# Kernel tuning notes

Measured on AMD Instinct MI355X. Metric: run time of the kernel, lower is better.

Reference implementation:

```python
import jax, jax.numpy as jnp
import numpy as np

EPS = 1e-5

def _ln(x, g, b):
    m = x.mean(-1, keepdims=True)
    v = jnp.var(x, axis=-1, keepdims=True)
    return (x - m) * jax.lax.rsqrt(v + EPS) * g + b

def _conv(x, w, b, stride=1, pad=1):
    y = jax.lax.conv_general_dilated(x, w, (stride, stride), [(pad, pad), (pad, pad)],
                                     dimension_numbers=('NCHW', 'OIHW', 'NCHW'))
    return y + b[None, :, None, None]

def _bn(x, g, b, m, v):
    # inference-mode BatchNorm2d
    inv = jax.lax.rsqrt(v + EPS)
    return (x - m[None, :, None, None]) * (g * inv)[None, :, None, None] + b[None, :, None, None]

def _sru_dir(u0, u1, u2, res, vf, vr, bf, br, reverse):
    # elementwise gated recurrence (SRU v2, identity activation, no dropout)
    def step(c, inp):
        a0, a1, a2, rx = inp
        f = jax.nn.sigmoid(a1 + vf * c + bf)
        c2 = f * c + (1.0 - f) * a0
        r = jax.nn.sigmoid(a2 + vr * c2 + br)
        return c2, r * c2 + (1.0 - r) * rx
    c0 = jnp.zeros_like(u0[0])
    _, hs = jax.lax.scan(step, c0, (u0, u1, u2, res), reverse=reverse)
    return hs

def _sru_layer(x, g, b, wp, w, vc, bias, k, h):
    # x: [L,B,n_in]; layer_norm on input, factored weight (projection), bidirectional
    xn = _ln(x, g, b)
    L, B, _ = xn.shape
    U = (xn @ wp) @ w                      # [L,B,2*k*h]
    U = U.reshape(L, B, 2, k, h)
    outs = []
    for d, rev in ((0, False), (1, True)):
        u = U[:, :, d]
        res = u[..., 3, :] if k == 4 else xn[..., d * h:(d + 1) * h]
        outs.append(_sru_dir(u[..., 0, :], u[..., 1, :], u[..., 2, :], res,
                             vc[d, 0], vc[d, 1], bias[d, 0], bias[d, 1], rev))
    return jnp.concatenate(outs, axis=-1)

def _forward(x, conv0_w, conv0_b, rconv1_w, rconv1_b, rbn1_g, rbn1_b, rbn1_m, rbn1_v,
             rconv2_w, rconv2_b, rbn2_g, rbn2_b, rbn2_m, rbn2_v,
             ln0_g, ln0_b, wproj0, w0, vc0, bias0, ln_g, ln_b, wproj, w, vc, bias,
             cln_g, cln_b, cls_w):
    H = 512
    h = _conv(x, conv0_w, conv0_b, stride=2)           # [B,32,F/2,T/2]
    for i in range(3):                                  # 3 residual blocks
        r = h
        h1 = jax.nn.relu(_bn(_conv(h, rconv1_w[i], rconv1_b[i]), rbn1_g[i], rbn1_b[i], rbn1_m[i], rbn1_v[i]))
        h2 = _bn(_conv(h1, rconv2_w[i], rconv2_b[i]), rbn2_g[i], rbn2_b[i], rbn2_m[i], rbn2_v[i])
        h = jax.nn.relu(h2 + r)
    Bb, C, Fr, Tt = h.shape
    s = h.reshape(Bb, C * Fr, Tt).transpose(2, 0, 1)   # [T,B,2048]
    s = _sru_layer(s, ln0_g, ln0_b, wproj0, w0, vc0, bias0, 4, H)  # layer 0: n_in != n_out -> k=4
    for i in range(3):                                  # layers 1..3: n_in == n_out -> k=3
        s = _sru_layer(s, ln_g[i], ln_b[i], wproj[i], w[i], vc[i], bias[i], 3, H)
    s = s.transpose(1, 0, 2)                            # [B,T,1024]
    s = _ln(s, cln_g, cln_b)
    return s @ cls_w                                    # [B,T,30]

def setup_inputs():
    key = jax.random.key(0)
    ks = iter(jax.random.split(key, 32))
    def nrm(shape, scale=1.0):
        return jax.random.normal(next(ks), shape, jnp.float32) * scale
    H, P, F2, D, hb = 512, 256, 2048, 1024, -2.0
    d = {}
    d['x'] = nrm((16, 1, 128, 2048))
    d['conv0_w'] = nrm((32, 1, 3, 3), (2.0 / 9) ** 0.5)
    d['conv0_b'] = jnp.zeros((32,))
    d['rconv1_w'] = nrm((3, 32, 32, 3, 3), (2.0 / (32 * 9)) ** 0.5)
    d['rconv1_b'] = jnp.zeros((3, 32))
    d['rbn1_g'] = jnp.ones((3, 32)); d['rbn1_b'] = jnp.zeros((3, 32))
    d['rbn1_m'] = nrm((3, 32), 0.1); d['rbn1_v'] = jnp.ones((3, 32))
    d['rconv2_w'] = nrm((3, 32, 32, 3, 3), (2.0 / (32 * 9)) ** 0.5)
    d['rconv2_b'] = jnp.zeros((3, 32))
    d['rbn2_g'] = 0.1 * jnp.ones((3, 32)); d['rbn2_b'] = jnp.zeros((3, 32))
    d['rbn2_m'] = nrm((3, 32), 0.1); d['rbn2_v'] = jnp.ones((3, 32))
    d['ln0_g'] = jnp.ones((F2,)); d['ln0_b'] = jnp.zeros((F2,))
    d['wproj0'] = nrm((F2, P), F2 ** -0.5)
    d['w0'] = nrm((P, 2 * 4 * H), P ** -0.5)
    d['vc0'] = nrm((2, 2, H), 0.1)
    d['bias0'] = jnp.zeros((2, 2, H)).at[:, 0].set(hb)
    d['ln_g'] = jnp.ones((3, D)); d['ln_b'] = jnp.zeros((3, D))
    d['wproj'] = nrm((3, D, P), D ** -0.5)
    d['w'] = nrm((3, P, 2 * 3 * H), P ** -0.5)
    d['vc'] = nrm((3, 2, 2, H), 0.1)
    d['bias'] = jnp.zeros((3, 2, 2, H)).at[:, :, 0].set(hb)
    d['cln_g'] = jnp.ones((D,)); d['cln_b'] = jnp.zeros((D,))
    d['cls_w'] = nrm((D, 30), D ** -0.5)
    return d

def reference(x, conv0_w, conv0_b, rconv1_w, rconv1_b, rbn1_g, rbn1_b, rbn1_m, rbn1_v,
              rconv2_w, rconv2_b, rbn2_g, rbn2_b, rbn2_m, rbn2_v,
              ln0_g, ln0_b, wproj0, w0, vc0, bias0, ln_g, ln_b, wproj, w, vc, bias,
              cln_g, cln_b, cls_w):
    return _forward(x, conv0_w, conv0_b, rconv1_w, rconv1_b, rbn1_g, rbn1_b, rbn1_m, rbn1_v,
                    rconv2_w, rconv2_b, rbn2_g, rbn2_b, rbn2_m, rbn2_v,
                    ln0_g, ln0_b, wproj0, w0, vc0, bias0, ln_g, ln_b, wproj, w, vc, bias,
                    cln_g, cln_b, cls_w)
```

## Files before the change

### kernel.cpp

```cpp
#include <hip/hip_runtime.h>
#include <hip/hip_bf16.h>
#include <math.h>

#define DEV __device__ __forceinline__

typedef __attribute__((ext_vector_type(8))) short short8;
typedef __attribute__((ext_vector_type(4))) float floatx4;

DEV float b2f_lo(unsigned u) { return __uint_as_float(u << 16); }
DEV float b2f_hi(unsigned u) { return __uint_as_float(u & 0xffff0000u); }

#if __has_builtin(__builtin_amdgcn_exp2f)
DEV float fexp2_(float x) { return __builtin_amdgcn_exp2f(x); }
#else
DEV float fexp2_(float x) { return exp2f(x); }
#endif
#if __has_builtin(__builtin_amdgcn_rcpf)
DEV float frcp_(float x) { return __builtin_amdgcn_rcpf(x); }
#else
DEV float frcp_(float x) { return 1.f / x; }
#endif

DEV void gl2lds16(const void* g, void* l) {
  __builtin_amdgcn_global_load_lds(
      (const __attribute__((address_space(1))) unsigned int*)g,
      (__attribute__((address_space(3))) unsigned int*)l, 16, 0, 0);
}

union U8 { uint4 u; __hip_bfloat16 h[8]; };

DEV int swz64(int x)    { return (x & ~63) | ((x & 15) << 2) | ((x >> 4) & 3); }
DEV int invswz64(int x) { return (x & ~63) | ((x & 3) << 4) | ((x >> 2) & 15); }

__global__ __launch_bounds__(256) void conv_stem_nhwc(const float* __restrict__ x,
    const float* __restrict__ w, const float* __restrict__ bias,
    __hip_bfloat16* __restrict__ out) {
  __shared__ float sX[3][2052];
  __shared__ float sW[288];
  __shared__ float sB[32];
  const int tid = threadIdx.x;
  const int f = blockIdx.x, n = blockIdx.y;
  const float* xb = x + (size_t)n * 262144;

  for (int i = tid; i < 1536; i += 256) {
    int r = i >> 9, c4 = i & 511;
    int fi = 2 * f - 1 + r;
    float4 v = {0.f, 0.f, 0.f, 0.f};
    if (fi >= 0 && fi < 128) v = *(const float4*)&xb[fi * 2048 + c4 * 4];
    sX[r][1 + c4 * 4 + 0] = v.x;
    sX[r][1 + c4 * 4 + 1] = v.y;
    sX[r][1 + c4 * 4 + 2] = v.z;
    sX[r][1 + c4 * 4 + 3] = v.w;
  }
  if (tid < 3) { sX[tid][0] = 0.f; sX[tid][2049] = 0.f; }
  for (int i = tid; i < 288; i += 256) sW[i] = w[i];
  if (tid < 32) sB[tid] = bias[tid];
  __syncthreads();

  float xv[4][9];
#pragma unroll
  for (int q = 0; q < 4; ++q) {
    int t = tid + q * 256;
#pragma unroll
    for (int r = 0; r < 3; ++r)
#pragma unroll
      for (int dc = 0; dc < 3; ++dc)
        xv[q][r * 3 + dc] = sX[r][2 * t + dc];
  }
#pragma unroll
  for (int ocq = 0; ocq < 4; ++ocq) {
    float wr[8][9];
#pragma unroll
    for (int oo = 0; oo < 8; ++oo)
#pragma unroll
      for (int qq = 0; qq < 9; ++qq)
        wr[oo][qq] = sW[(ocq * 8 + oo) * 9 + qq];
#pragma unroll
    for (int q = 0; q < 4; ++q) {
      U8 o;
#pragma unroll
      for (int oo = 0; oo < 8; ++oo) {
        float acc = sB[ocq * 8 + oo];
#pragma unroll
        for (int qq = 0; qq < 9; ++qq) acc = fmaf(wr[oo][qq], xv[q][qq], acc);
        o.h[oo] = __float2bfloat16(acc);
      }
      int t = tid + q * 256;
      *(uint4*)&out[(((size_t)n * 64 + f) * 1024 + t) * 32 + ocq * 8] = o.u;
    }
  }
}

__global__ __launch_bounds__(256) void wtap_conv6(const float* __restrict__ w1,
    const float* __restrict__ w2, __hip_bfloat16* __restrict__ out) {
  int i = blockIdx.x * 256 + threadIdx.x;
  if (i < 55296) {
    int b = i / 9216, r = i - b * 9216;
    int layer = b >> 1, which = b & 1;
    const float* src = (which ? w2 : w1) + layer * 9216;
    int tap = r >> 10, oc = (r >> 5) & 31, ic = r & 31;
    out[b * 9216 + r] = __float2bfloat16(src[(oc * 32 + ic) * 9 + tap]);
  }
}

template <int ADD>
__global__ __launch_bounds__(256) void conv_mfma(const __hip_bfloat16* __restrict__ Hin,
    const __hip_bfloat16* __restrict__ wt,
    const float* __restrict__ cb, const float* __restrict__ bg,
    const float* __restrict__ bb, const float* __restrict__ bm,
    const float* __restrict__ bv, __hip_bfloat16* Hres) {
  __shared__ __hip_bfloat16 sIn[6 * 66 * 40];
  __hip_bfloat16* sOut = sIn;
  const int tid = threadIdx.x;
  const int tb = blockIdx.x, fb = blockIdx.y, n = blockIdx.z;
  const int t0 = tb * 64, f0 = fb * 4;
  const __hip_bfloat16* Hb = Hin + (size_t)n * 2097152;

  for (int c = tid; c < 1584; c += 256) {
    int rr = c / 264;
    int r2 = c - rr * 264;
    int p = r2 >> 2, icq = r2 & 3;
    int fi = f0 - 1 + rr;
    int tg = t0 + p - 1;
    uint4 v = {0, 0, 0, 0};
    if (fi >= 0 && fi < 64 && tg >= 0 && tg < 1024)
      v = *(const uint4*)&Hb[((size_t)fi * 1024 + tg) * 32 + icq * 8];
    *(uint4*)&sIn[(rr * 66 + p) * 40 + icq * 8] = v;
  }

  const int lane = tid & 63, wave = tid >> 6;
  const int fr = lane & 15, fq = lane >> 4;
  short8 bfrag[9][2];
#pragma unroll
  for (int tap = 0; tap < 9; ++tap)
#pragma unroll
    for (int j = 0; j < 2; ++j)
      bfrag[tap][j] = *(const short8*)&wt[(tap * 32 + j * 16 + fr) * 32 + fq * 8];

  __syncthreads();

  const int tw = wave * 16;
  floatx4 acc[4][2];
#pragma unroll
  for (int fp = 0; fp < 4; ++fp)
#pragma unroll
    for (int j = 0; j < 2; ++j) acc[fp][j] = (floatx4){0.f, 0.f, 0.f, 0.f};

#pragma unroll
  for (int fp = 0; fp < 4; ++fp) {
    int pbase = tw + fr;
#pragma unroll
    for (int df = 0; df < 3; ++df)
#pragma unroll
      for (int dc = 0; dc < 3; ++dc) {
        short8 af =
            *(const short8*)&sIn[((fp + df) * 66 + pbase + dc) * 40 + fq * 8];
        acc[fp][0] = __builtin_amdgcn_mfma_f32_16x16x32_bf16(
            af, bfrag[df * 3 + dc][0], acc[fp][0], 0, 0, 0);
        acc[fp][1] = __builtin_amdgcn_mfma_f32_16x16x32_bf16(
            af, bfrag[df * 3 + dc][1], acc[fp][1], 0, 0, 0);
      }
  }

  float sc0 = bg[fr] * rsqrtf(bv[fr] + 1e-5f);
  float sh0 = (cb[fr] - bm[fr]) * sc0 + bb[fr];
  float sc1 = bg[fr + 16] * rsqrtf(bv[fr + 16] + 1e-5f);
  float sh1 = (cb[fr + 16] - bm[fr + 16]) * sc1 + bb[fr + 16];

  __syncthreads();
#pragma unroll
  for (int fp = 0; fp < 4; ++fp)
#pragma unroll
    for (int j = 0; j < 2; ++j) {
      float sc = j ? sc1 : sc0, sh = j ? sh1 : sh0;
#pragma unroll
      for (int reg = 0; reg < 4; ++reg) {
        int t_l = tw + fq * 4 + reg;
        sOut[(fp * 64 + t_l) * 40 + j * 16 + fr] =
            __float2bfloat16(acc[fp][j][reg] * sc + sh);
      }
    }
  __syncthreads();

  for (int c = tid; c < 1024; c += 256) {
    int fp = c >> 8, rem = c & 255;
    int t_l = rem >> 2, icq = rem & 3;
    U8 y;
    y.u = *(uint4*)&sOut[(fp * 64 + t_l) * 40 + icq * 8];
    size_t addr = (((size_t)n * 64 + f0 + fp) * 1024 + t0 + t_l) * 32 + icq * 8;
    U8 o;
    if (ADD) {
      U8 r;
      r.u = *(const uint4*)&Hres[addr];
#pragma unroll
      for (int i = 0; i < 8; ++i)
        o.h[i] = __float2bfloat16(
            fmaxf(__bfloat162float(y.h[i]) + __bfloat162float(r.h[i]), 0.f));
    } else {
#pragma unroll
      for (int i = 0; i < 8; ++i)
        o.h[i] = __float2bfloat16(fmaxf(__bfloat162float(y.h[i]), 0.f));
    }
    *(uint4*)&Hres[addr] = o.u;
  }
}

__global__ __launch_bounds__(256) void ln_nhwc(const __hip_bfloat16* __restrict__ H,
    const float* __restrict__ g, const float* __restrict__ b,
    __hip_bfloat16* __restrict__ xn) {
  int r = blockIdx.x;
  int t = r >> 4, n = r & 15;
  int tid = threadIdx.x;
  int f = tid >> 2, icq = tid & 3;
  U8 v;
  v.u = *(const uint4*)&H[(((size_t)n * 64 + f) * 1024 + t) * 32 + icq * 8];
  float xv[8];
  float sum = 0.f, ss = 0.f;
#pragma unroll
  for (int i = 0; i < 8; ++i) {
    xv[i] = __bfloat162float(v.h[i]);
    sum += xv[i];
    ss += xv[i] * xv[i];
  }
#pragma unroll
  for (int off = 32; off > 0; off >>= 1) {
    sum += __shfl_down(sum, off);
    ss  += __shfl_down(ss, off);
  }
  __shared__ float red[8];
  int lane = tid & 63, wave = tid >> 6;
  if (lane == 0) { red[wave] = sum; red[4 + wave] = ss; }
  __syncthreads();
  sum = red[0] + red[1] + red[2] + red[3];
  ss  = red[4] + red[5] + red[6] + red[7];
  float mean = sum * (1.f / 2048.f);
  float var = ss * (1.f / 2048.f) - mean * mean;
  float inv = rsqrtf(var + 1e-5f);
  U8 o;
#pragma unroll
  for (int i = 0; i < 8; ++i) {
    int cf = (icq * 8 + i) * 64 + f;
    o.h[i] = __float2bfloat16((xv[i] - mean) * inv * g[cf] + b[cf]);
  }
  *(uint4*)&xn[(size_t)r * 2048 + tid * 8] = o.u;
}

__global__ __launch_bounds__(256) void wt_perm0(const float* __restrict__ in,
    __hip_bfloat16* __restrict__ out) {
  int i = blockIdx.x * 256 + threadIdx.x;
  int p = i >> 11, kp = i & 2047;
  int ic = kp & 31, f = kp >> 5;
  out[i] = __float2bfloat16(in[(ic * 64 + f) * 256 + p]);
}

__global__ __launch_bounds__(256) void wt_bf16(const float* __restrict__ in,
    __hip_bfloat16* __restrict__ out, int K, int N, int inStride, int outStride) {
  __shared__ float tile[32][33];
  int x = threadIdx.x, y0 = threadIdx.y;
  int bn = blockIdx.x * 32;
  int bk = blockIdx.y * 32;
  const float* src = in + (size_t)blockIdx.z * inStride;
  __hip_bfloat16* dst = out + (size_t)blockIdx.z * outStride;
#pragma unroll
  for (int i = 0; i < 4; ++i) {
    int yy = y0 + i * 8;
    tile[yy][x] = src[(size_t)(bk + yy) * N + bn + x];
  }
  __syncthreads();
#pragma unroll
  for (int i = 0; i < 4; ++i) {
    int yy = y0 + i * 8;
    dst[(size_t)(bn + yy) * K + bk + x] = __float2bfloat16(tile[x][yy]);
  }
}

__global__ void wexp_prep(const float* __restrict__ in,
    __hip_bfloat16* __restrict__ out, int korig, int inStride, int outStride) {
  __shared__ float tile[32][33];
  int jt = blockIdx.x;
  int ckt = blockIdx.y;
  int z = blockIdx.z;
  int layer = z >> 3, dk = z & 7;
  int d = dk >> 2, k = dk & 3;
  if (k >= korig) return;
  const float* src = in + (size_t)layer * inStride;
  __hip_bfloat16* dst = out + (size_t)layer * outStride;
  int x = threadIdx.x, y0 = threadIdx.y;
#pragma unroll
  for (int i = 0; i < 4; ++i) {
    int yy = y0 + i * 8;
    tile[yy][x] = src[(size_t)(ckt * 32 + yy) * (korig * 1024) +
                      (d * korig + k) * 512 + jt * 32 + x];
  }
  __syncthreads();
#pragma unroll
  for (int i = 0; i < 4; ++i) {
    int yy = y0 + i * 8;
    int ch = d * 512 + jt * 32 + yy;
    int rOld;
    if (korig == 4)
      rOld = (k < 2) ? (ch * 2 + k) : (2048 + ch * 2 + (k - 2));
    else
      rOld = (k < 2) ? (ch * 2 + k) : (2048 + ch);
    int rNew = invswz64(rOld);
    int ckp = swz64(ckt * 32 + x);
    dst[(size_t)rNew * 256 + ckp] = __float2bfloat16(tile[x][yy]);
  }
}

__global__ __launch_bounds__(256) void colsb_prep(const float* __restrict__ bias0,
    const float* __restrict__ bias3, float2* __restrict__ out) {
  int i = blockIdx.x * 256 + threadIdx.x;
  if (i >= 13312) return;
  const float NL2E = -1.44269504f;
  float s = 1.f, bb = 0.f;
  if (i < 4096) {
    int col = i;
    if (col < 2048) {
      int ch = col >> 1, e = col & 1;
      int d = ch >> 9, jj = ch & 511;
      if (e) { s = NL2E; bb = NL2E * bias0[d * 1024 + jj]; }
    } else {
      int cc = col - 2048, ch = cc >> 1, e = cc & 1;
      int d = ch >> 9, jj = ch & 511;
      if (!e) { s = NL2E; bb = NL2E * bias0[d * 1024 + 512 + jj]; }
    }
  } else {
    int rem = i - 4096;
    int layer = rem / 3072, col = rem - layer * 3072;
    const float* bsrc = bias3 + layer * 2048;
    if (col < 2048) {
      int ch = col >> 1, e = col & 1;
      int d = ch >> 9, jj = ch & 511;
      if (e) { s = NL2E; bb = NL2E * bsrc[d * 1024 + jj]; }
    } else {
      int ch = col - 2048;
      int d = ch >> 9, jj = ch & 511;
      s = NL2E; bb = NL2E * bsrc[d * 1024 + 512 + jj];
    }
  }
  out[i] = make_float2(s, bb);
}

__global__ __launch_bounds__(256) void wct_prep(const float* __restrict__ in,
    __hip_bfloat16* __restrict__ out) {
  int i = blockIdx.x * 256 + threadIdx.x;
  int nn = i >> 10, kk = i & 1023;
  out[i] = __float2bfloat16(nn < 30 ? in[kk * 30 + nn] : 0.f);
}

__global__ __launch_bounds__(256) void gemm_bf16(const __hip_bfloat16* __restrict__ A,
    const __hip_bfloat16* __restrict__ Bt, __hip_bfloat16* __restrict__ C,
    const float2* __restrict__ csb, int M, int N, int K) {
  __shared__ __hip_bfloat16 As[128 * 32];
  __shared__ __hip_bfloat16 Bs[128 * 32];
  const int tid = threadIdx.x;
  const int gx = gridDim.x;
  const int nwg = gx * gridDim.y;
  const int bid = blockIdx.y * gx + blockIdx.x;
  const int wgid = (bid & 7) * (nwg >> 3) + (bid >> 3);
  const int m0 = (wgid / gx) * 128, n0 = (wgid % gx) * 128;
  const int lane = tid & 63, wave = tid >> 6;
  const int wm = wave & 1, wn = wave >> 1;
  const int fr = lane & 15, fq = lane >> 4;
  const int srow = lane >> 2, sch = lane & 3;

  const __hip_bfloat16* ga0 = &A[(size_t)(m0 + wave * 32 + srow) * K + sch * 8];
  const __hip_bfloat16* ga1 = ga0 + (size_t)16 * K;
  const __hip_bfloat16* gb0 = &Bt[(size_t)(n0 + wave * 32 + srow) * K + sch * 8];
  const __hip_bfloat16* gb1 = gb0 + (size_t)16 * K;
  __hip_bfloat16* la0 = &As[(wave * 32) * 32];
  __hip_bfloat16* la1 = &As[(wave * 32 + 16) * 32];
  __hip_bfloat16* lb0 = &Bs[(wave * 32) * 32];
  __hip_bfloat16* lb1 = &Bs[(wave * 32 + 16) * 32];

  floatx4 acc[4][4];
#pragma unroll
  for (int i = 0; i < 4; ++i)
#pragma unroll
    for (int j = 0; j < 4; ++j)
      acc[i][j] = (floatx4){0.f, 0.f, 0.f, 0.f};

  for (int k0 = 0; k0 < K; k0 += 32) {
    __syncthreads();
    gl2lds16(ga0 + k0, la0);
    gl2lds16(ga1 + k0, la1);
    gl2lds16(gb0 + k0, lb0);
    gl2lds16(gb1 + k0, lb1);
    __syncthreads();

    short8 af[4], bf_[4];
#pragma unroll
    for (int i = 0; i < 4; ++i) {
      af[i]  = *(const short8*)&As[(wm * 64 + i * 16 + fr) * 32 + fq * 8];
      bf_[i] = *(const short8*)&Bs[(wn * 64 + i * 16 + fr) * 32 + fq * 8];
    }
#pragma unroll
    for (int i = 0; i < 4; ++i)
#pragma unroll
      for (int j = 0; j < 4; ++j)
        acc[i][j] = __builtin_amdgcn_mfma_f32_16x16x32_bf16(af[i], bf_[j],
                                                            acc[i][j], 0, 0, 0);
  }

  const int p0 = n0 + wn * 64 + fr * 4;
  float s0 = 1.f, s1 = 1.f, s2 = 1.f, s3 = 1.f;
  float c0 = 0.f, c1 = 0.f, c2v = 0.f, c3 = 0.f;
  if (csb) {
    float2 t0 = csb[p0], t1 = csb[p0 + 1], t2 = csb[p0 + 2], t3 = csb[p0 + 3];
    s0 = t0.x; c0 = t0.y; s1 = t1.x; c1 = t1.y;
    s2 = t2.x; c2v = t2.y; s3 = t3.x; c3 = t3.y;
  }
#pragma unroll
  for (int i = 0; i < 4; ++i)
#pragma unroll
    for (int reg = 0; reg < 4; ++reg) {
      int row = m0 + wm * 64 + i * 16 + fq * 4 + reg;
      union { uint2 u; __hip_bfloat16 h[4]; } o;
      o.h[0] = __float2bfloat16(fmaf(acc[i][0][reg], s0, c0));
      o.h[1] = __float2bfloat16(fmaf(acc[i][1][reg], s1, c1));
      o.h[2] = __float2bfloat16(fmaf(acc[i][2][reg], s2, c2v));
      o.h[3] = __float2bfloat16(fmaf(acc[i][3][reg], s3, c3));
      *(uint2*)&C[(size_t)row * N + p0] = o.u;
    }
}

__global__ __launch_bounds__(256) void cls_gemm(const __hip_bfloat16* __restrict__ A,
    const __hip_bfloat16* __restrict__ Wct, float* __restrict__ out) {
  const int tid = threadIdx.x;
  const int lane = tid & 63, wave = tid >> 6;
  const int fr = lane & 15, fq = lane >> 4;
  const int m0 = (blockIdx.x * 4 + wave) * 16;
  floatx4 acc[2];
  acc[0] = (floatx4){0.f, 0.f, 0.f, 0.f};
  acc[1] = (floatx4){0.f, 0.f, 0.f, 0.f};
#pragma unroll 4
  for (int k0 = 0; k0 < 1024; k0 += 32) {
    short8 af = *(const short8*)&A[(size_t)(m0 + fr) * 1024 + k0 + fq * 8];
    short8 b0 = *(const short8*)&Wct[(size_t)fr * 1024 + k0 + fq * 8];
    short8 b1 = *(const short8*)&Wct[(size_t)(16 + fr) * 1024 + k0 + fq * 8];
    acc[0] = __builtin_amdgcn_mfma_f32_16x16x32_bf16(af, b0, acc[0], 0, 0, 0);
    acc[1] = __builtin_amdgcn_mfma_f32_16x16x32_bf16(af, b1, acc[1], 0, 0, 0);
  }
#pragma unroll
  for (int j = 0; j < 2; ++j) {
    int col = j * 16 + fr;
    if (col < 30) {
#pragma unroll
      for (int reg = 0; reg < 4; ++reg) {
        int row = m0 + fq * 4 + reg;
        int t = row >> 4, n = row & 15;
        out[(size_t)n * 30720 + t * 30 + col] = acc[j][reg];
      }
    }
  }
}

template <int ROWB>
__global__ __launch_bounds__(64) void scan_c(const __hip_bfloat16* __restrict__ U,
    const float* __restrict__ vc, __hip_bfloat16* __restrict__ c2out) {
  int gid = blockIdx.x * 64 + threadIdx.x;
  int j = gid & 511;
  int n = (gid >> 9) & 15;
  int d = gid >> 13;
  const float NL2E = -1.44269504f;
  float vf2 = NL2E * vc[d * 1024 + j];

  const char* Ub = (const char*)U + (size_t)n * ROWB + (size_t)(d * 512 + j) * 4;
  char* Ob = (char*)c2out + (size_t)n * 2048 + (size_t)(d * 512 + j) * 2;
  const int US = d ? -(16 * ROWB) : (16 * ROWB);
  const int OS = d ? -32768 : 32768;
  int uoff = d ? 1023 * 16 * ROWB : 0;
  int ooff = d ? 1023 * 32768 : 0;

  uint B0[16], B1[16], B2[16], B3[16];
  float c = 0.f;

#define LOADC(UB)                                                         \
  {                                                                       \
    _Pragma("unroll") for (int ss = 0; ss < 16; ++ss) {                   \
      UB[ss] = *(const uint*)(Ub + uoff);                                 \
      uoff += US;                                                         \
    }                                                                     \
  }

#define COMPC(UB)                                                         \
  {                                                                       \
    _Pragma("unroll") for (int ss = 0; ss < 16; ++ss) {                   \
      uint u = UB[ss];                                                    \
      float a0 = b2f_lo(u), a1p = b2f_hi(u);                              \
      float f = frcp_(1.f + fexp2_(fmaf(vf2, c, a1p)));                   \
      c = fmaf(f, c - a0, a0);                                            \
      *(__hip_bfloat16*)(Ob + ooff) = __float2bfloat16(c);                \
      ooff += OS;                                                         \
    }                                                                     \
  }

  LOADC(B0);
  LOADC(B1);
  LOADC(B2);
  for (int cb = 0; cb < 64; cb += 4) {
    LOADC(B3);
    COMPC(B0);
    if (cb + 4 < 64) LOADC(B0);
    COMPC(B1);
    if (cb + 5 < 64) LOADC(B1);
    COMPC(B2);
    if (cb + 6 < 64) LOADC(B2);
    COMPC(B3);
  }
#undef LOADC
#undef COMPC
}

template <int K4>
__global__ __launch_bounds__(256) void yln(const __hip_bfloat16* __restrict__ c2buf,
    const __hip_bfloat16* __restrict__ U, const __hip_bfloat16* __restrict__ xn,
    const float* __restrict__ vc, const float* __restrict__ g,
    const float* __restrict__ b, __hip_bfloat16* __restrict__ outx) {
  int r = blockIdx.x;
  int tid = threadIdx.x;
  int ch0 = tid * 4;
  const float NL2E = -1.44269504f;

  union { ushort4 u; __hip_bfloat16 h[4]; } cv;
  cv.u = *(const ushort4*)&c2buf[(size_t)r * 1024 + ch0];
  float a2p[4], rx[4];
  if (K4) {
    uint4 pr = *(const uint4*)((const char*)U + (size_t)r * 8192 + 4096 + tid * 16);
    uint pp[4] = {pr.x, pr.y, pr.z, pr.w};
#pragma unroll
    for (int i = 0; i < 4; ++i) { a2p[i] = b2f_lo(pp[i]); rx[i] = b2f_hi(pp[i]); }
  } else {
    union { ushort4 u; __hip_bfloat16 h[4]; } av, xv;
    av.u = *(const ushort4*)((const char*)U + (size_t)r * 6144 + 4096 + tid * 8);
    xv.u = *(const ushort4*)&xn[(size_t)r * 1024 + ch0];
#pragma unroll
    for (int i = 0; i < 4; ++i) {
      a2p[i] = __bfloat162float(av.h[i]);
      rx[i]  = __bfloat162float(xv.h[i]);
    }
  }

  int d = ch0 >> 9, j0 = ch0 & 511;
  float y[4], sum = 0.f, ss = 0.f;
#pragma unroll
  for (int i = 0; i < 4; ++i) {
    float vr2 = NL2E * vc[d * 1024 + 512 + j0 + i];
    float cc = __bfloat162float(cv.h[i]);
    float rr = frcp_(1.f + fexp2_(fmaf(vr2, cc, a2p[i])));
    y[i] = fmaf(rr, cc - rx[i], rx[i]);
    sum += y[i];
    ss += y[i] * y[i];
  }
#pragma unroll
  for (int off = 32; off > 0; off >>= 1) {
    sum += __shfl_down(sum, off);
    ss  += __shfl_down(ss, off);
  }
  __shared__ float red[8];
  int lane = tid & 63, wave = tid >> 6;
  if (lane == 0) { red[wave] = sum; red[4 + wave] = ss; }
  __syncthreads();
  sum = red[0] + red[1] + red[2] + red[3];
  ss  = red[4] + red[5] + red[6] + red[7];
  float mean = sum * (1.f / 1024.f);
  float var = ss * (1.f / 1024.f) - mean * mean;
  float inv = rsqrtf(var + 1e-5f);
  float4 gv = *(const float4*)&g[ch0];
  float4 bv = *(const float4*)&b[ch0];
  float gg[4] = {gv.x, gv.y, gv.z, gv.w};
  float bb[4] = {bv.x, bv.y, bv.z, bv.w};
  union { ushort4 u; __hip_bfloat16 h[4]; } o;
#pragma unroll
  for (int i = 0; i < 4; ++i)
    o.h[i] = __float2bfloat16((y[i] - mean) * inv * gg[i] + bb[i]);
  *(ushort4*)&outx[(size_t)r * 1024 + ch0] = o.u;
}

extern "C" void kernel_launch(void* const* d_in, const int* in_sizes, int n_in,
                              void* d_out, int out_size, void* d_ws, size_t ws_size,
                              hipStream_t stream) {
  const float* x        = (const float*)d_in[0];
  const float* conv0_w  = (const float*)d_in[1];
  const float* conv0_b  = (const float*)d_in[2];
  const float* rconv1_w = (const float*)d_in[3];
  const float* rconv1_b = (const float*)d_in[4];
  const float* rbn1_g   = (const float*)d_in[5];
  const float* rbn1_b   = (const float*)d_in[6];
  const float* rbn1_m   = (const float*)d_in[7];
  const float* rbn1_v   = (const float*)d_in[8];
  const float* rconv2_w = (const float*)d_in[9];
  const float* rconv2_b = (const float*)d_in[10];
  const float* rbn2_g   = (const float*)d_in[11];
  const float* rbn2_b   = (const float*)d_in[12];
  const float* rbn2_m   = (const float*)d_in[13];
  const float* rbn2_v   = (const float*)d_in[14];
  const float* ln0_g    = (const float*)d_in[15];
  const float* ln0_b    = (const float*)d_in[16];
  const float* wproj0   = (const float*)d_in[17];
  const float* w0       = (const float*)d_in[18];
  const float* vc0      = (const float*)d_in[19];
  const float* bias0    = (const float*)d_in[20];
  const float* ln_g     = (const float*)d_in[21];
  const float* ln_b     = (const float*)d_in[22];
  const float* wproj    = (const float*)d_in[23];
  const float* w        = (const float*)d_in[24];
  const float* vc       = (const float*)d_in[25];
  const float* bias     = (const float*)d_in[26];
  const float* cln_g    = (const float*)d_in[27];
  const float* cln_b    = (const float*)d_in[28];
  const float* cls_w    = (const float*)d_in[29];
  float* out = (float*)d_out;

  float* Af = (float*)d_ws;
  float* Bf = Af + 33554432;
  __hip_bfloat16* Ah = (__hip_bfloat16*)Af;
  __hip_bfloat16* Bh = (__hip_bfloat16*)Bf;

  __hip_bfloat16* hA     = Ah;
  __hip_bfloat16* hB     = Bh;
  __hip_bfloat16* wt_all = Ah + 62914560;
  __hip_bfloat16* Wp0t   = Ah + 52428800;

  __hip_bfloat16* c2   = Bh;
  __hip_bfloat16* xnc  = Bh + 16777216;
  __hip_bfloat16* xn3  = Bh + 33554432;
  __hip_bfloat16* tmp  = Bh + 50331648;
  __hip_bfloat16* W3p  = Bh + 54525952;
  __hip_bfloat16* W0p  = Bh + 57671680;
  __hip_bfloat16* Wpt3 = Bh + 58720256;
  float2* csb          = (float2*)(Bh + 59506688);
  __hip_bfloat16* xn0  = Bh;
  __hip_bfloat16* U    = Ah;
  __hip_bfloat16* Wct  = Ah;

  const float2* csb4 = csb;
  const float2* csb3 = csb + 4096;

  wtap_conv6<<<216, 256, 0, stream>>>(rconv1_w, rconv2_w, wt_all);
  wt_perm0<<<2048, 256, 0, stream>>>(wproj0, Wp0t);
  wexp_prep<<<dim3(16, 8, 8), dim3(32, 8), 0, stream>>>(w0, W0p, 4, 0, 0);
  wexp_prep<<<dim3(16, 8, 24), dim3(32, 8), 0, stream>>>(w, W3p, 3,
                                                         786432, 786432);
  wt_bf16<<<dim3(8, 32, 3), dim3(32, 8), 0, stream>>>(wproj, Wpt3, 1024, 256,
                                                      262144, 262144);
  colsb_prep<<<52, 256, 0, stream>>>(bias0, bias, csb);

  conv_stem_nhwc<<<dim3(64, 16), 256, 0, stream>>>(x, conv0_w, conv0_b, hA);
  for (int i = 0; i < 3; ++i) {
    conv_mfma<0><<<dim3(16, 16, 16), 256, 0, stream>>>(hA, wt_all + (i * 2) * 9216,
        rconv1_b + i * 32, rbn1_g + i * 32, rbn1_b + i * 32,
        rbn1_m + i * 32, rbn1_v + i * 32, hB);
    conv_mfma<1><<<dim3(16, 16, 16), 256, 0, stream>>>(hB, wt_all + (i * 2 + 1) * 9216,
        rconv2_b + i * 32, rbn2_g + i * 32, rbn2_b + i * 32,
        rbn2_m + i * 32, rbn2_v + i * 32, hA);
  }

  ln_nhwc<<<16384, 256, 0, stream>>>(hA, ln0_g, ln0_b, xn0);
  gemm_bf16<<<dim3(2, 128), 256, 0, stream>>>(xn0, Wp0t, tmp, nullptr,
                                              16384, 256, 2048);
  gemm_bf16<<<dim3(32, 128), 256, 0, stream>>>(tmp, W0p, U, csb4,
                                               16384, 4096, 256);
  scan_c<8192><<<256, 64, 0, stream>>>(U, vc0, c2);
  __hip_bfloat16* xnA = xn3;
  __hip_bfloat16* xnB = xnc;
  yln<1><<<16384, 256, 0, stream>>>(c2, U, nullptr, vc0, ln_g, ln_b, xnA);

  for (int i = 0; i < 3; ++i) {
    gemm_bf16<<<dim3(2, 128), 256, 0, stream>>>(xnA, Wpt3 + i * 262144, tmp,
                                                nullptr, 16384, 256, 1024);
    gemm_bf16<<<dim3(24, 128), 256, 0, stream>>>(tmp, W3p + i * 786432, U,
                                                 csb3 + i * 3072, 16384, 3072, 256);
    scan_c<6144><<<256, 64, 0, stream>>>(U, vc + i * 2048, c2);
    const float* gg = (i < 2) ? (ln_g + (i + 1) * 1024) : cln_g;
    const float* bb = (i < 2) ? (ln_b + (i + 1) * 1024) : cln_b;
    yln<0><<<16384, 256, 0, stream>>>(c2, U, xnA, vc + i * 2048, gg, bb, xnB);
    __hip_bfloat16* sw = xnA; xnA = xnB; xnB = sw;
  }

  wct_prep<<<128, 256, 0, stream>>>(cls_w, Wct);
  cls_gemm<<<256, 256, 0, stream>>>(xnA, Wct, out);
}
```

Measured before the change: 1.035 ms.

## Load GEMM MFMA fragments directly from global memory with register double buffering

The bf16 GEMM no longer stages A and B tiles through LDS with global_load_lds and two barriers per K step. Each wave now loads its MFMA operand fragments straight from global memory into registers, using two register sets so the next K slice is fetched while the current one is multiplied. This removes LDS traffic and block-wide synchronisation. In exchange each fragment is fetched redundantly by the waves that share it, global accesses become 16-byte strided reads across rows, and the loop assumes K is a multiple of 64.

```diff
diff --git a/kernel.cpp b/kernel.cpp
--- a/kernel.cpp
+++ b/kernel.cpp
@@ -20,12 +20,6 @@
 #else
 DEV float frcp_(float x) { return 1.f / x; }
 #endif
-
-DEV void gl2lds16(const void* g, void* l) {
-  __builtin_amdgcn_global_load_lds(
-      (const __attribute__((address_space(1))) unsigned int*)g,
-      (__attribute__((address_space(3))) unsigned int*)l, 16, 0, 0);
-}
 
 union U8 { uint4 u; __hip_bfloat16 h[8]; };
 
@@ -352,8 +346,6 @@
 __global__ __launch_bounds__(256) void gemm_bf16(const __hip_bfloat16* __restrict__ A,
     const __hip_bfloat16* __restrict__ Bt, __hip_bfloat16* __restrict__ C,
     const float2* __restrict__ csb, int M, int N, int K) {
-  __shared__ __hip_bfloat16 As[128 * 32];
-  __shared__ __hip_bfloat16 Bs[128 * 32];
   const int tid = threadIdx.x;
   const int gx = gridDim.x;
   const int nwg = gx * gridDim.y;
@@ -363,16 +355,14 @@
   const int lane = tid & 63, wave = tid >> 6;
   const int wm = wave & 1, wn = wave >> 1;
   const int fr = lane & 15, fq = lane >> 4;
-  const int srow = lane >> 2, sch = lane & 3;
-
-  const __hip_bfloat16* ga0 = &A[(size_t)(m0 + wave * 32 + srow) * K + sch * 8];
-  const __hip_bfloat16* ga1 = ga0 + (size_t)16 * K;
-  const __hip_bfloat16* gb0 = &Bt[(size_t)(n0 + wave * 32 + srow) * K + sch * 8];
-  const __hip_bfloat16* gb1 = gb0 + (size_t)16 * K;
-  __hip_bfloat16* la0 = &As[(wave * 32) * 32];
-  __hip_bfloat16* la1 = &As[(wave * 32 + 16) * 32];
-  __hip_bfloat16* lb0 = &Bs[(wave * 32) * 32];
-  __hip_bfloat16* lb1 = &Bs[(wave * 32 + 16) * 32];
+
+  const __hip_bfloat16* pa[4];
+  const __hip_bfloat16* pb[4];
+#pragma unroll
+  for (int i = 0; i < 4; ++i) {
+    pa[i] = &A[(size_t)(m0 + wm * 64 + i * 16 + fr) * K + fq * 8];
+    pb[i] = &Bt[(size_t)(n0 + wn * 64 + i * 16 + fr) * K + fq * 8];
+  }
 
   floatx4 acc[4][4];
 #pragma unroll
@@ -381,27 +371,32 @@
     for (int j = 0; j < 4; ++j)
       acc[i][j] = (floatx4){0.f, 0.f, 0.f, 0.f};
 
-  for (int k0 = 0; k0 < K; k0 += 32) {
-    __syncthreads();
-    gl2lds16(ga0 + k0, la0);
-    gl2lds16(ga1 + k0, la1);
-    gl2lds16(gb0 + k0, lb0);
-    gl2lds16(gb1 + k0, lb1);
-    __syncthreads();
-
-    short8 af[4], bf_[4];
-#pragma unroll
-    for (int i = 0; i < 4; ++i) {
-      af[i]  = *(const short8*)&As[(wm * 64 + i * 16 + fr) * 32 + fq * 8];
-      bf_[i] = *(const short8*)&Bs[(wn * 64 + i * 16 + fr) * 32 + fq * 8];
-    }
-#pragma unroll
-    for (int i = 0; i < 4; ++i)
-#pragma unroll
-      for (int j = 0; j < 4; ++j)
-        acc[i][j] = __builtin_amdgcn_mfma_f32_16x16x32_bf16(af[i], bf_[j],
-                                                            acc[i][j], 0, 0, 0);
-  }
+  short8 aC[4], bC[4], aN[4], bN[4];
+
+#define LOADF(AA, BB, kk)                                                 \
+  {                                                                       \
+    _Pragma("unroll") for (int i = 0; i < 4; ++i) {                       \
+      AA[i] = *(const short8*)(pa[i] + (kk));                             \
+      BB[i] = *(const short8*)(pb[i] + (kk));                             \
+    }                                                                     \
+  }
+#define MFMA16(AA, BB)                                                    \
+  {                                                                       \
+    _Pragma("unroll") for (int i = 0; i < 4; ++i)                         \
+    _Pragma("unroll") for (int j = 0; j < 4; ++j)                         \
+      acc[i][j] = __builtin_amdgcn_mfma_f32_16x16x32_bf16(                \
+          AA[i], BB[j], acc[i][j], 0, 0, 0);                              \
+  }
+
+  LOADF(aC, bC, 0);
+  for (int k = 0; k < K; k += 64) {
+    LOADF(aN, bN, k + 32);
+    MFMA16(aC, bC);
+    if (k + 64 < K) LOADF(aC, bC, k + 64);
+    MFMA16(aN, bN);
+  }
+#undef LOADF
+#undef MFMA16
 
   const int p0 = n0 + wn * 64 + fr * 4;
   float s0 = 1.f, s1 = 1.f, s2 = 1.f, s3 = 1.f;
```

New measurement: 1.290 ms. +24.6%, slower.

## Double-buffer LDS tiles in bf16 GEMM to overlap global loads with MFMA

Applied to the files above, without the earlier changes.

Splits the GEMM's shared-memory A and B tiles into two buffers. The next K-slice is loaded directly into LDS while the current slice is computed, with vmcnt waits and barriers sequencing the two. This hides global-load latency behind matrix-core work. The cost is twice the LDS per block, which may lower occupancy. The loop also assumes K is a multiple of 64, and relies on hand-placed wait counts being correct.

```diff
diff --git a/kernel.cpp b/kernel.cpp
--- a/kernel.cpp
+++ b/kernel.cpp
@@ -352,8 +352,8 @@
 __global__ __launch_bounds__(256) void gemm_bf16(const __hip_bfloat16* __restrict__ A,
     const __hip_bfloat16* __restrict__ Bt, __hip_bfloat16* __restrict__ C,
     const float2* __restrict__ csb, int M, int N, int K) {
-  __shared__ __hip_bfloat16 As[128 * 32];
-  __shared__ __hip_bfloat16 Bs[128 * 32];
+  __shared__ __hip_bfloat16 As[2][128 * 32];
+  __shared__ __hip_bfloat16 Bs[2][128 * 32];
   const int tid = threadIdx.x;
   const int gx = gridDim.x;
   const int nwg = gx * gridDim.y;
@@ -369,10 +369,8 @@
   const __hip_bfloat16* ga1 = ga0 + (size_t)16 * K;
   const __hip_bfloat16* gb0 = &Bt[(size_t)(n0 + wave * 32 + srow) * K + sch * 8];
   const __hip_bfloat16* gb1 = gb0 + (size_t)16 * K;
-  __hip_bfloat16* la0 = &As[(wave * 32) * 32];
-  __hip_bfloat16* la1 = &As[(wave * 32 + 16) * 32];
-  __hip_bfloat16* lb0 = &Bs[(wave * 32) * 32];
-  __hip_bfloat16* lb1 = &Bs[(wave * 32 + 16) * 32];
+  const int lo0 = (wave * 32) * 32;
+  const int lo1 = (wave * 32 + 16) * 32;
 
   floatx4 acc[4][4];
 #pragma unroll
@@ -381,27 +379,49 @@
     for (int j = 0; j < 4; ++j)
       acc[i][j] = (floatx4){0.f, 0.f, 0.f, 0.f};
 
-  for (int k0 = 0; k0 < K; k0 += 32) {
-    __syncthreads();
-    gl2lds16(ga0 + k0, la0);
-    gl2lds16(ga1 + k0, la1);
-    gl2lds16(gb0 + k0, lb0);
-    gl2lds16(gb1 + k0, lb1);
-    __syncthreads();
-
-    short8 af[4], bf_[4];
-#pragma unroll
-    for (int i = 0; i < 4; ++i) {
-      af[i]  = *(const short8*)&As[(wm * 64 + i * 16 + fr) * 32 + fq * 8];
-      bf_[i] = *(const short8*)&Bs[(wn * 64 + i * 16 + fr) * 32 + fq * 8];
-    }
-#pragma unroll
-    for (int i = 0; i < 4; ++i)
-#pragma unroll
-      for (int j = 0; j < 4; ++j)
-        acc[i][j] = __builtin_amdgcn_mfma_f32_16x16x32_bf16(af[i], bf_[j],
-                                                            acc[i][j], 0, 0, 0);
-  }
+#define STAGE(BUF, kk)                                                    \
+  {                                                                       \
+    gl2lds16(ga0 + (kk), &As[BUF][lo0]);                                  \
+    gl2lds16(ga1 + (kk), &As[BUF][lo1]);                                  \
+    gl2lds16(gb0 + (kk), &Bs[BUF][lo0]);                                  \
+    gl2lds16(gb1 + (kk), &Bs[BUF][lo1]);                                  \
+  }
+#define COMPUTE(BUF)                                                      \
+  {                                                                       \
+    short8 af[4], bf_[4];                                                 \
+    _Pragma("unroll") for (int i = 0; i < 4; ++i) {                       \
+      af[i]  = *(const short8*)&As[BUF][(wm * 64 + i * 16 + fr) * 32 + fq * 8]; \
+      bf_[i] = *(const short8*)&Bs[BUF][(wn * 64 + i * 16 + fr) * 32 + fq * 8]; \
+    }                                                                     \
+    _Pragma("unroll") for (int i = 0; i < 4; ++i)                         \
+      _Pragma("unroll") for (int j = 0; j < 4; ++j)                       \
+        acc[i][j] = __builtin_amdgcn_mfma_f32_16x16x32_bf16(              \
+            af[i], bf_[j], acc[i][j], 0, 0, 0);                           \
+  }
+#define CFENCE asm volatile("" ::: "memory")
+
+  STAGE(0, 0);
+  for (int k0 = 0; k0 < K; k0 += 64) {
+    STAGE(1, k0 + 32);
+    asm volatile("s_waitcnt vmcnt(4)" ::: "memory");
+    __builtin_amdgcn_s_barrier();
+    COMPUTE(0);
+    CFENCE;
+    __builtin_amdgcn_s_barrier();
+    if (k0 + 64 < K) {
+      STAGE(0, k0 + 64);
+      asm volatile("s_waitcnt vmcnt(4)" ::: "memory");
+    } else {
+      asm volatile("s_waitcnt vmcnt(0)" ::: "memory");
+    }
+    __builtin_amdgcn_s_barrier();
+    COMPUTE(1);
+    CFENCE;
+    __builtin_amdgcn_s_barrier();
+  }
+#undef STAGE
+#undef COMPUTE
+#undef CFENCE
 
   const int p0 = n0 + wn * 64 + fr * 4;
   float s0 = 1.f, s1 = 1.f, s2 = 1.f, s3 = 1.f;
```

After: 1.006 ms. 1.03x faster.
